# Performance work log

Measured on AMD Instinct MI355X. Metric: run time of the kernel, lower is better.

## Reference

```python
import jax, jax.numpy as jnp
import numpy as np

EPS = 1e-5
B, HD, LD, OD, E = 4, 256, 512, 256, 64  # E = out_dim // reduction
H, W, H2, W2 = 64, 64, 32, 32

def conv1x1(x, Wt, b=None):
    # x: [B,C,H,W], Wt: [O,C]
    y = jnp.einsum('bchw,oc->bohw', x, Wt)
    if b is not None:
        y = y + b[None, :, None, None]
    return y

def bn(x, s, bi, m, v):
    # eval-mode BatchNorm2d with running stats
    inv = (s / jnp.sqrt(v + EPS))[None, :, None, None]
    return (x - m[None, :, None, None]) * inv + bi[None, :, None, None]

def setup_inputs() -> dict:
    key = jax.random.key(0)
    ks = jax.random.split(key, 24)
    def n(k, shape, scale=0.05):
        return jax.random.normal(k, shape, dtype=jnp.float32) * scale
    inp = {
        'high_feat': jax.random.normal(ks[0], (B, HD, H, W), dtype=jnp.float32),
        'low_feat': jax.random.normal(ks[1], (B, LD, H2, W2), dtype=jnp.float32),
        'W_high': n(ks[2], (E, HD)),
        'bn_h_scale': 1.0 + n(ks[3], (E,)), 'bn_h_bias': n(ks[4], (E,)),
        'bn_h_mean': n(ks[5], (E,)), 'bn_h_var': 0.5 + jax.random.uniform(ks[6], (E,), dtype=jnp.float32),
        'W_low': n(ks[7], (E, LD)),
        'bn_l_scale': 1.0 + n(ks[8], (E,)), 'bn_l_bias': n(ks[9], (E,)),
        'bn_l_mean': n(ks[10], (E,)), 'bn_l_var': 0.5 + jax.random.uniform(ks[11], (E,), dtype=jnp.float32),
        'W_q': n(ks[12], (E, E)), 'b_q': n(ks[13], (E,)),
        'W_k': n(ks[14], (E, E)), 'b_k': n(ks[15], (E,)),
        'W_vh': n(ks[16], (OD, HD)), 'b_vh': n(ks[17], (OD,)),
        'W_vl': n(ks[18], (OD, LD)), 'b_vl': n(ks[19], (OD,)),
        'W_out': n(ks[20], (OD, 2 * OD)),
        'bn_o_scale': 1.0 + n(ks[21], (OD,)), 'bn_o_bias': n(ks[22], (OD,)),
        'bn_o_mean': jnp.zeros((OD,), jnp.float32), 'bn_o_var': jnp.ones((OD,), jnp.float32),
        'gamma': n(ks[23], (1,), scale=0.5),
    }
    return inp

def reference(high_feat, low_feat, W_high, bn_h_scale, bn_h_bias, bn_h_mean, bn_h_var,
              W_low, bn_l_scale, bn_l_bias, bn_l_mean, bn_l_var,
              W_q, b_q, W_k, b_k, W_vh, b_vh, W_vl, b_vl,
              W_out, bn_o_scale, bn_o_bias, bn_o_mean, bn_o_var, gamma):
    N = H * W
    # bilinear upsample low_feat to high_feat spatial size (align_corners=False)
    low = jax.image.resize(low_feat, (B, LD, H, W), method='bilinear')
    he = jax.nn.relu(bn(conv1x1(high_feat, W_high), bn_h_scale, bn_h_bias, bn_h_mean, bn_h_var))
    le = jax.nn.relu(bn(conv1x1(low, W_low), bn_l_scale, bn_l_bias, bn_l_mean, bn_l_var))
    q = conv1x1(he, W_q, b_q).reshape(B, E, N)   # [B,E,N1]
    k = conv1x1(le, W_k, b_k).reshape(B, E, N)   # [B,E,N2]
    energy = jnp.einsum('bcn,bcm->bnm', q, k)    # [B,N1,N2]
    attn = jax.nn.softmax(energy, axis=-1)
    vh = conv1x1(high_feat, W_vh, b_vh).reshape(B, OD, N)
    vl = conv1x1(low, W_vl, b_vl).reshape(B, OD, N)
    out_high = jnp.einsum('bcm,bnm->bcn', vh, attn).reshape(B, OD, H, W)
    out_low = jnp.einsum('bcn,bnm->bcm', vl, attn).reshape(B, OD, H, W)
    cat = jnp.concatenate([out_high, out_low], axis=1)  # [B,2*OD,H,W]
    out = jax.nn.relu(bn(conv1x1(cat, W_out), bn_o_scale, bn_o_bias, bn_o_mean, bn_o_var))
    return high_feat + gamma[0] * out
```

## Files before the change

### kernel.cpp

```cpp
#include <hip/hip_runtime.h>
#include <hip/hip_bf16.h>

#define B_   4
#define HD_  256
#define LD_  512
#define OD_  256
#define E_   64
#define N_   4096
#define N2_  1024
#define EPS_ 1e-5f

typedef __hip_bfloat16 bf16;
typedef __attribute__((ext_vector_type(8))) short short8;
typedef __attribute__((ext_vector_type(4))) float floatx4;

#define MFMA16(a, b, c) __builtin_amdgcn_mfma_f32_16x16x32_bf16(a, b, c, 0, 0, 0)

#define GLOAD(dst, ptr) \
  asm volatile("global_load_dwordx4 %0, %1, off" : "=v"(dst) : "v"(ptr) : "memory")
#define VWAIT() do { \
  asm volatile("s_waitcnt vmcnt(0)" ::: "memory"); \
  __builtin_amdgcn_sched_barrier(0); \
} while (0)

#define WH_OFF   0
#define WL_OFF   16384
#define WQ_OFF   49152
#define WK_OFF   53248
#define WVH_OFF  57344
#define WVL_OFF  122880
#define WO_OFF   253952
#define WTOT     385024

__device__ __forceinline__ unsigned short f2b_bits(float f) {
  union { float f; unsigned int u; } cv; cv.f = f;
  unsigned int u = cv.u;
  return (unsigned short)((u + 0x7FFFu + ((u >> 16) & 1u)) >> 16);
}
__device__ __forceinline__ float bits2f(unsigned short h) {
  union { unsigned int u; float f; } cv; cv.u = ((unsigned int)h) << 16;
  return cv.f;
}
__device__ __forceinline__ float ldext(const void* p, size_t i, int fl) {
  if (fl) return __bfloat162float(((const bf16*)p)[i]);
  return ((const float*)p)[i];
}
__device__ __forceinline__ short8 ld8(const short* p) { return *(const short8*)p; }
__device__ __forceinline__ short8 i4s8(int4 v) {
  union { int4 i; short8 s; } u; u.i = v; return u.s;
}
__device__ __forceinline__ short8 ldP(const unsigned short* row, int off) {
  ushort4 a = *(const ushort4*)(row + off);
  ushort4 b = *(const ushort4*)(row + off + 4);
  short8 r;
  r[0] = (short)a.x; r[1] = (short)a.y; r[2] = (short)a.z; r[3] = (short)a.w;
  r[4] = (short)b.x; r[5] = (short)b.y; r[6] = (short)b.z; r[7] = (short)b.w;
  return r;
}

__device__ __forceinline__ size_t frag_off(int r, int k, int K) {
  return ((size_t)(r >> 4) * ((size_t)K << 4)) + ((size_t)(k >> 5) << 9)
       + ((r & 15) << 5) + (k & 31);
}
__device__ __forceinline__ size_t v_off(int c, int m) {
  return ((size_t)(m >> 5) << 13) + ((c >> 4) << 9) + (((m >> 3) & 3) << 7)
       + ((c & 15) << 3) + (m & 7);
}

__global__ void detect_dtype_k(const void* probe, int* dflag) {
  if (threadIdx.x == 0 && blockIdx.x == 0) {
    const unsigned int* u = (const unsigned int*)probe;
    int bf = 1;
    for (int i = 0; i < 32; i++)
      if (u[i] != 0x3F803F80u) bf = 0;
    dflag[0] = bf;
  }
}

__global__ __launch_bounds__(256) void cvt_weights_k(
    const void* Wh, const void* Wl, const void* Wq, const void* Wk,
    const void* Wvh, const void* Wvl, const void* Wo,
    unsigned short* wbuf, const int* dflag)
{
  const int fl = dflag[0];
  int i = blockIdx.x * 256 + threadIdx.x;
  if (i >= WTOT) return;
  const void* src; int li, off, ksh;
  if      (i < WL_OFF)  { src = Wh;  li = i - WH_OFF;  off = WH_OFF;  ksh = 8; }
  else if (i < WQ_OFF)  { src = Wl;  li = i - WL_OFF;  off = WL_OFF;  ksh = 9; }
  else if (i < WK_OFF)  { src = Wq;  li = i - WQ_OFF;  off = WQ_OFF;  ksh = 6; }
  else if (i < WVH_OFF) { src = Wk;  li = i - WK_OFF;  off = WK_OFF;  ksh = 6; }
  else if (i < WVL_OFF) { src = Wvh; li = i - WVH_OFF; off = WVH_OFF; ksh = 8; }
  else if (i < WO_OFF)  { src = Wvl; li = i - WVL_OFF; off = WVL_OFF; ksh = 9; }
  else                  { src = Wo;  li = i - WO_OFF;  off = WO_OFF;  ksh = 9; }
  int K = 1 << ksh;
  int r = li >> ksh, k = li & (K - 1);
  wbuf[off + frag_off(r, k, K)] = f2b_bits(ldext(src, li, fl));
}

__global__ __launch_bounds__(256) void transpose_cvt_k(
    const void* X, unsigned short* Xt, int C, int S, const int* dflag)
{
  __shared__ unsigned short T[64][66];
  const int fl = dflag[0];
  const int tid = threadIdx.x;
  const int s0 = blockIdx.x * 64, c0 = blockIdx.y * 64, b = blockIdx.z;
  const size_t ibase = (size_t)b * C * S;
  const size_t obase = (size_t)b * S * C;
  const int sl = tid & 63, q = tid >> 6;
  for (int i = 0; i < 16; i++) {
    int c = q + i * 4;
    T[c][sl] = f2b_bits(ldext(X, ibase + (size_t)(c0 + c) * S + s0 + sl, fl));
  }
  __syncthreads();
  for (int i = 0; i < 16; i++) {
    int s = q + i * 4;
    Xt[obase + frag_off(s0 + s, c0 + sl, C)] = T[sl][s];
  }
}

__global__ __launch_bounds__(256) void gemm_k(
    const unsigned short* A, long sA,
    const unsigned short* Bm, long sB,
    unsigned short* D, long sD, int ldd,
    int K, int mode, int axis, int swz,
    const void* p0, const void* p1, const void* p2, const void* p3,
    const int* dflag)
{
  const int fl = dflag[0];
  const int tid = threadIdx.x;
  const int w = tid >> 6, lane = tid & 63;
  const int g = lane >> 4, c16 = lane & 15;
  const int r0 = blockIdx.x * 64 + (w >> 1) * 32;
  const int c0 = blockIdx.y * 64 + (w & 1) * 32;
  const short* Ab = (const short*)A + (size_t)blockIdx.z * sA;
  const short* Bb = (const short*)Bm + (size_t)blockIdx.z * sB;
  unsigned short* Db = D + (size_t)blockIdx.z * sD;

  floatx4 acc[2][2];
  #pragma unroll
  for (int i = 0; i < 2; i++)
    #pragma unroll
    for (int j = 0; j < 2; j++) acc[i][j] = (floatx4){0.f, 0.f, 0.f, 0.f};

  for (int k0 = 0; k0 < K; k0 += 64) {
    short8 Af[2][2], Bf[2][2];
    #pragma unroll
    for (int t = 0; t < 2; t++)
      #pragma unroll
      for (int kc = 0; kc < 2; kc++) {
        Af[t][kc] = ld8(Ab + frag_off(r0 + t * 16 + c16, k0 + kc * 32 + g * 8, K));
        Bf[t][kc] = ld8(Bb + frag_off(c0 + t * 16 + c16, k0 + kc * 32 + g * 8, K));
      }
    #pragma unroll
    for (int kc = 0; kc < 2; kc++)
      #pragma unroll
      for (int rt = 0; rt < 2; rt++)
        #pragma unroll
        for (int ct = 0; ct < 2; ct++)
          acc[rt][ct] = MFMA16(Af[rt][kc], Bf[ct][kc], acc[rt][ct]);
  }

  #pragma unroll
  for (int rt = 0; rt < 2; rt++)
    #pragma unroll
    for (int ct = 0; ct < 2; ct++)
      #pragma unroll
      for (int r = 0; r < 4; r++) {
        int rr = r0 + rt * 16 + g * 4 + r;
        int cc = c0 + ct * 16 + c16;
        int pi = axis ? rr : cc;
        float v = acc[rt][ct][r];
        if (mode == 1) v += ldext(p0, pi, fl);
        else if (mode >= 2) {
          float inv = ldext(p0, pi, fl) * rsqrtf(ldext(p3, pi, fl) + EPS_);
          v = v * inv + (ldext(p1, pi, fl) - ldext(p2, pi, fl) * inv);
          if (mode == 3) v = fmaxf(v, 0.f);
        }
        size_t idx;
        if (swz == 1)      idx = frag_off(rr, cc, ldd);
        else if (swz == 2) idx = v_off(rr, cc);
        else               idx = (size_t)rr * ldd + cc;
        Db[idx] = f2b_bits(v);
      }
}

__global__ __launch_bounds__(256) void upsample_rows_k(
    const unsigned short* src, unsigned short* dst, int relu)
{
  int idx = blockIdx.x * 256 + threadIdx.x;
  int e = idx & 63, n = (idx >> 6) & (N_ - 1), b = idx >> 18;
  int y = n >> 6, x = n & 63;
  int y0 = (y - 1) >> 1;  float wy = (y & 1) ? 0.25f : 0.75f;
  int x0 = (x - 1) >> 1;  float wx = (x & 1) ? 0.25f : 0.75f;
  int y0c = max(y0, 0), y1c = min(y0 + 1, 31);
  int x0c = max(x0, 0), x1c = min(x0 + 1, 31);
  const unsigned short* sb = src + ((size_t)b * N2_) * 64 + e;
  float v00 = bits2f(sb[(y0c * 32 + x0c) * 64]), v01 = bits2f(sb[(y0c * 32 + x1c) * 64]);
  float v10 = bits2f(sb[(y1c * 32 + x0c) * 64]), v11 = bits2f(sb[(y1c * 32 + x1c) * 64]);
  float v = (1.f - wy) * ((1.f - wx) * v00 + wx * v01)
          + wy * ((1.f - wx) * v10 + wx * v11);
  if (relu) v = fmaxf(v, 0.f);
  dst[(size_t)b * N_ * 64 + frag_off(n, e, 64)] = f2b_bits(v);
}

__global__ __launch_bounds__(256) void upsample_swz_k(
    const unsigned short* src, unsigned short* dst)
{
  int idx = blockIdx.x * 256 + threadIdx.x;
  int n = idx & (N_ - 1), c = (idx >> 12) & 255, b = idx >> 20;
  int y = n >> 6, x = n & 63;
  int y0 = (y - 1) >> 1;  float wy = (y & 1) ? 0.25f : 0.75f;
  int x0 = (x - 1) >> 1;  float wx = (x & 1) ? 0.25f : 0.75f;
  int y0c = max(y0, 0), y1c = min(y0 + 1, 31);
  int x0c = max(x0, 0), x1c = min(x0 + 1, 31);
  const unsigned short* sb = src + (size_t)(b * 256 + c) * N2_;
  float v00 = bits2f(sb[y0c * 32 + x0c]), v01 = bits2f(sb[y0c * 32 + x1c]);
  float v10 = bits2f(sb[y1c * 32 + x0c]), v11 = bits2f(sb[y1c * 32 + x1c]);
  float v = (1.f - wy) * ((1.f - wx) * v00 + wx * v01)
          + wy * ((1.f - wx) * v10 + wx * v11);
  dst[(size_t)b * 256 * N_ + v_off(c, n)] = f2b_bits(v);
}


__global__ __launch_bounds__(256, 4) void attn_apply_high_mfma_k(
    const bf16* qt, const bf16* kt, const bf16* vh,
    float* lsum_p, unsigned short* ohp0, unsigned short* ohp1)
{
  __shared__ __align__(16) unsigned short Pb[2][32][132];
  __shared__ float Lw[4][32];
  const int tid = threadIdx.x;
  const int w = tid >> 6, lane = tid & 63;
  const int g = lane >> 4, c16 = lane & 15;
  const int L = blockIdx.x;
  const int b = (L & 7) >> 1;
  const int n0 = (L >> 3) * 32;
  const int half = L & 1;
  const int mbase = half * 2048, mend = mbase + 2048;
  const short* q = (const short*)qt + (size_t)b * N_ * E_;
  const short* k = (const short*)kt + (size_t)b * N_ * E_;
  const short* v = (const short*)vh + (size_t)b * OD_ * N_;

  short8 Aq[2][2];
  #pragma unroll
  for (int nt = 0; nt < 2; nt++)
    #pragma unroll
    for (int ks = 0; ks < 2; ks++)
      Aq[nt][ks] = ld8(q + frag_off(n0 + nt * 16 + c16, ks * 32 + g * 8, 64));

  float lsum[2][4] = {};
  floatx4 oacc[2][4];
  #pragma unroll
  for (int nt = 0; nt < 2; nt++)
    #pragma unroll
    for (int ct = 0; ct < 4; ct++)
      oacc[nt][ct] = (floatx4){0.f, 0.f, 0.f, 0.f};

  short8 BkC[2][2];
  #pragma unroll
  for (int mt = 0; mt < 2; mt++)
    #pragma unroll
    for (int ks = 0; ks < 2; ks++)
      BkC[mt][ks] = ld8(k + frag_off(mbase + w * 32 + mt * 16 + c16, ks * 32 + g * 8, 64));

  int buf = 0;
  for (int m0 = mbase; m0 < mend; m0 += 128, buf ^= 1) {
    int4 bv[8];
    #pragma unroll
    for (int ks = 0; ks < 2; ks++)
      #pragma unroll
      for (int ct = 0; ct < 4; ct++)
        GLOAD(bv[ks * 4 + ct],
              (v + v_off(w * 64 + ct * 16 + c16, m0 + ks * 32 + g * 8)));
    floatx4 s[2][2];
    #pragma unroll
    for (int nt = 0; nt < 2; nt++)
      #pragma unroll
      for (int mt = 0; mt < 2; mt++) {
        floatx4 z = (floatx4){0.f, 0.f, 0.f, 0.f};
        z = MFMA16(Aq[nt][0], BkC[mt][0], z);
        z = MFMA16(Aq[nt][1], BkC[mt][1], z);
        s[nt][mt] = z;
      }
    int mn_ = m0 + 128;
    if (mn_ < mend) {
      #pragma unroll
      for (int mt = 0; mt < 2; mt++)
        #pragma unroll
        for (int ks = 0; ks < 2; ks++)
          BkC[mt][ks] = ld8(k + frag_off(mn_ + w * 32 + mt * 16 + c16, ks * 32 + g * 8, 64));
    }
    #pragma unroll
    for (int nt = 0; nt < 2; nt++)
      #pragma unroll
      for (int mt = 0; mt < 2; mt++)
        #pragma unroll
        for (int r = 0; r < 4; r++) {
          float p = __expf(fminf(s[nt][mt][r], 60.f));
          lsum[nt][r] += p;
          Pb[buf][nt * 16 + g * 4 + r][w * 32 + mt * 16 + c16] = f2b_bits(p);
        }
    __syncthreads();
    VWAIT();
    #pragma unroll
    for (int ks = 0; ks < 2; ks++) {
      short8 Ap0 = ldP(&Pb[buf][c16][0],      ks * 32 + g * 8);
      short8 Ap1 = ldP(&Pb[buf][16 + c16][0], ks * 32 + g * 8);
      #pragma unroll
      for (int ct = 0; ct < 4; ct++) {
        short8 Bv = i4s8(bv[ks * 4 + ct]);
        oacc[0][ct] = MFMA16(Ap0, Bv, oacc[0][ct]);
        oacc[1][ct] = MFMA16(Ap1, Bv, oacc[1][ct]);
      }
    }
    #pragma unroll
    for (int ks = 0; ks < 2; ks++)
      #pragma unroll
      for (int ct = 0; ct < 4; ct++)
        GLOAD(bv[ks * 4 + ct],
              (v + v_off(w * 64 + ct * 16 + c16, m0 + (ks + 2) * 32 + g * 8)));
    VWAIT();
    #pragma unroll
    for (int ks = 0; ks < 2; ks++) {
      short8 Ap0 = ldP(&Pb[buf][c16][0],      (ks + 2) * 32 + g * 8);
      short8 Ap1 = ldP(&Pb[buf][16 + c16][0], (ks + 2) * 32 + g * 8);
      #pragma unroll
      for (int ct = 0; ct < 4; ct++) {
        short8 Bv = i4s8(bv[ks * 4 + ct]);
        oacc[0][ct] = MFMA16(Ap0, Bv, oacc[0][ct]);
        oacc[1][ct] = MFMA16(Ap1, Bv, oacc[1][ct]);
      }
    }
  }
  #pragma unroll
  for (int d = 1; d < 16; d <<= 1)
    #pragma unroll
    for (int nt = 0; nt < 2; nt++)
      #pragma unroll
      for (int r = 0; r < 4; r++)
        lsum[nt][r] += __shfl_xor(lsum[nt][r], d);
  if (c16 == 0)
    #pragma unroll
    for (int nt = 0; nt < 2; nt++)
      #pragma unroll
      for (int r = 0; r < 4; r++)
        Lw[w][nt * 16 + g * 4 + r] = lsum[nt][r];
  __syncthreads();
  if (tid < 32)
    lsum_p[(size_t)half * 16384 + (size_t)b * N_ + n0 + tid] =
        Lw[0][tid] + Lw[1][tid] + Lw[2][tid] + Lw[3][tid];
  unsigned short* op = (half ? ohp1 : ohp0) + (size_t)b * N_ * OD_;
  #pragma unroll
  for (int nt = 0; nt < 2; nt++)
    #pragma unroll
    for (int ct = 0; ct < 4; ct++)
      #pragma unroll
      for (int r = 0; r < 4; r++) {
        int n = n0 + nt * 16 + g * 4 + r;
        int c = w * 64 + ct * 16 + c16;
        op[frag_off(n, c, 256)] = f2b_bits(oacc[nt][ct][r]);
      }
}

__global__ __launch_bounds__(256) void reduce_high_k(
    const unsigned short* p0, const unsigned short* p1, const float* lsum_p,
    unsigned short* oh, float* rsumG)
{
  size_t i8 = ((size_t)blockIdx.x * 256 + threadIdx.x) * 8;
  int slab = (int)(i8 >> 20);
  int loc  = (int)(i8 & 0xFFFFF);
  int n = (loc >> 12) * 16 + ((loc >> 5) & 15);
  int row = slab * N_ + n;
  float l = lsum_p[row] + lsum_p[16384 + row];
  float ri = 1.0f / l;
  const unsigned short* a = p0 + i8;
  const unsigned short* b = p1 + i8;
  short8 o;
  #pragma unroll
  for (int i = 0; i < 8; i++)
    o[i] = (short)f2b_bits((bits2f(a[i]) + bits2f(b[i])) * ri);
  *(short8*)(oh + i8) = o;
  if ((loc & 31) == 0) rsumG[row] = l;
}

__global__ __launch_bounds__(256, 4) void attn_apply_low_mfma_k(
    const bf16* qt, const bf16* kt, const bf16* vl,
    const float* rsumG, unsigned short* olp0, unsigned short* olp1)
{
  __shared__ __align__(16) unsigned short Pb[2][32][132];
  const int tid = threadIdx.x;
  const int w = tid >> 6, lane = tid & 63;
  const int g = lane >> 4, c16 = lane & 15;
  const int L = blockIdx.x;
  const int b = (L & 7) >> 1;
  const int m0 = (L >> 3) * 32;
  const int half = L & 1;
  const int nbase = half * 2048, nend = nbase + 2048;
  const short* q = (const short*)qt + (size_t)b * N_ * E_;
  const short* k = (const short*)kt + (size_t)b * N_ * E_;
  const short* v = (const short*)vl + (size_t)b * OD_ * N_;

  short8 Ak[2][2];
  #pragma unroll
  for (int mt = 0; mt < 2; mt++)
    #pragma unroll
    for (int ks = 0; ks < 2; ks++)
      Ak[mt][ks] = ld8(k + frag_off(m0 + mt * 16 + c16, ks * 32 + g * 8, 64));

  floatx4 oacc[2][4];
  #pragma unroll
  for (int mt = 0; mt < 2; mt++)
    #pragma unroll
    for (int ct = 0; ct < 4; ct++)
      oacc[mt][ct] = (floatx4){0.f, 0.f, 0.f, 0.f};

  short8 BqC[2][2];
  float riC[2];
  #pragma unroll
  for (int nt = 0; nt < 2; nt++) {
    #pragma unroll
    for (int ks = 0; ks < 2; ks++)
      BqC[nt][ks] = ld8(q + frag_off(nbase + w * 32 + nt * 16 + c16, ks * 32 + g * 8, 64));
    riC[nt] = 1.0f / rsumG[(size_t)b * N_ + nbase + w * 32 + nt * 16 + c16];
  }

  int buf = 0;
  for (int nL = nbase; nL < nend; nL += 128, buf ^= 1) {
    int4 bv[8];
    #pragma unroll
    for (int ks = 0; ks < 2; ks++)
      #pragma unroll
      for (int ct = 0; ct < 4; ct++)
        GLOAD(bv[ks * 4 + ct],
              (v + v_off(w * 64 + ct * 16 + c16, nL + ks * 32 + g * 8)));
    floatx4 s[2][2];
    #pragma unroll
    for (int mt = 0; mt < 2; mt++)
      #pragma unroll
      for (int nt = 0; nt < 2; nt++) {
        floatx4 z = (floatx4){0.f, 0.f, 0.f, 0.f};
        z = MFMA16(Ak[mt][0], BqC[nt][0], z);
        z = MFMA16(Ak[mt][1], BqC[nt][1], z);
        s[mt][nt] = z;
      }
    float riU[2]; riU[0] = riC[0]; riU[1] = riC[1];
    int nn_ = nL + 128;
    if (nn_ < nend) {
      #pragma unroll
      for (int nt = 0; nt < 2; nt++) {
        #pragma unroll
        for (int ks = 0; ks < 2; ks++)
          BqC[nt][ks] = ld8(q + frag_off(nn_ + w * 32 + nt * 16 + c16, ks * 32 + g * 8, 64));
        riC[nt] = 1.0f / rsumG[(size_t)b * N_ + nn_ + w * 32 + nt * 16 + c16];
      }
    }
    #pragma unroll
    for (int mt = 0; mt < 2; mt++)
      #pragma unroll
      for (int nt = 0; nt < 2; nt++)
        #pragma unroll
        for (int r = 0; r < 4; r++)
          Pb[buf][mt * 16 + g * 4 + r][w * 32 + nt * 16 + c16] =
              f2b_bits(__expf(fminf(s[mt][nt][r], 60.f)) * riU[nt]);
    __syncthreads();
    VWAIT();
    #pragma unroll
    for (int ks = 0; ks < 2; ks++) {
      short8 Ap0 = ldP(&Pb[buf][c16][0],      ks * 32 + g * 8);
      short8 Ap1 = ldP(&Pb[buf][16 + c16][0], ks * 32 + g * 8);
      #pragma unroll
      for (int ct = 0; ct < 4; ct++) {
        short8 Bv = i4s8(bv[ks * 4 + ct]);
        oacc[0][ct] = MFMA16(Ap0, Bv, oacc[0][ct]);
        oacc[1][ct] = MFMA16(Ap1, Bv, oacc[1][ct]);
      }
    }
    #pragma unroll
    for (int ks = 0; ks < 2; ks++)
      #pragma unroll
      for (int ct = 0; ct < 4; ct++)
        GLOAD(bv[ks * 4 + ct],
              (v + v_off(w * 64 + ct * 16 + c16, nL + (ks + 2) * 32 + g * 8)));
    VWAIT();
    #pragma unroll
    for (int ks = 0; ks < 2; ks++) {
      short8 Ap0 = ldP(&Pb[buf][c16][0],      (ks + 2) * 32 + g * 8);
      short8 Ap1 = ldP(&Pb[buf][16 + c16][0], (ks + 2) * 32 + g * 8);
      #pragma unroll
      for (int ct = 0; ct < 4; ct++) {
        short8 Bv = i4s8(bv[ks * 4 + ct]);
        oacc[0][ct] = MFMA16(Ap0, Bv, oacc[0][ct]);
        oacc[1][ct] = MFMA16(Ap1, Bv, oacc[1][ct]);
      }
    }
  }
  unsigned short* op = (half ? olp1 : olp0) + (size_t)b * N_ * OD_;
  #pragma unroll
  for (int mt = 0; mt < 2; mt++)
    #pragma unroll
    for (int ct = 0; ct < 4; ct++)
      #pragma unroll
      for (int r = 0; r < 4; r++) {
        int m = m0 + mt * 16 + g * 4 + r;
        int c = w * 64 + ct * 16 + c16;
        op[frag_off(m, c, 256)] = f2b_bits(oacc[mt][ct][r]);
      }
}

__global__ __launch_bounds__(256) void reduce_low_k(
    const unsigned short* p0, const unsigned short* p1, unsigned short* ol)
{
  size_t i8 = ((size_t)blockIdx.x * 256 + threadIdx.x) * 8;
  const unsigned short* a = p0 + i8;
  const unsigned short* b = p1 + i8;
  short8 o;
  #pragma unroll
  for (int i = 0; i < 8; i++)
    o[i] = (short)f2b_bits(bits2f(a[i]) + bits2f(b[i]));
  *(short8*)(ol + i8) = o;
}

__global__ __launch_bounds__(256) void final_mfma_k(
    const unsigned short* Wo, const unsigned short* oh, const unsigned short* ol,
    const void* sc, const void* bi, const void* mn, const void* vr,
    const void* hf, const void* gamma, void* out, const int* dflag)
{
  const int fl = dflag[0];
  const int tid = threadIdx.x;
  const int w = tid >> 6, lane = tid & 63;
  const int g = lane >> 4, c16 = lane & 15;
  const int r0 = blockIdx.x * 64 + (w >> 1) * 32;
  const int c0 = blockIdx.y * 64 + (w & 1) * 32;
  const int b = blockIdx.z;

  floatx4 acc[2][2];
  #pragma unroll
  for (int i = 0; i < 2; i++)
    #pragma unroll
    for (int j = 0; j < 2; j++) acc[i][j] = (floatx4){0.f, 0.f, 0.f, 0.f};

  #pragma unroll
  for (int half = 0; half < 2; half++) {
    const short* Bb = (const short*)(half ? ol : oh) + (size_t)b * N_ * 256;
    for (int k0 = 0; k0 < 256; k0 += 64) {
      short8 Af[2][2], Bf[2][2];
      #pragma unroll
      for (int t = 0; t < 2; t++)
        #pragma unroll
        for (int kc = 0; kc < 2; kc++) {
          Af[t][kc] = ld8((const short*)Wo + frag_off(r0 + t * 16 + c16,
                          half * 256 + k0 + kc * 32 + g * 8, 512));
          Bf[t][kc] = ld8(Bb + frag_off(c0 + t * 16 + c16, k0 + kc * 32 + g * 8, 256));
        }
      #pragma unroll
      for (int kc = 0; kc < 2; kc++)
        #pragma unroll
        for (int rt = 0; rt < 2; rt++)
          #pragma unroll
          for (int ct = 0; ct < 2; ct++)
            acc[rt][ct] = MFMA16(Af[rt][kc], Bf[ct][kc], acc[rt][ct]);
    }
  }

  float gm = ldext(gamma, 0, fl);
  #pragma unroll
  for (int rt = 0; rt < 2; rt++)
    #pragma unroll
    for (int r = 0; r < 4; r++) {
      int o = r0 + rt * 16 + g * 4 + r;
      float inv = ldext(sc, o, fl) * rsqrtf(ldext(vr, o, fl) + EPS_);
      float bb = ldext(bi, o, fl) - ldext(mn, o, fl) * inv;
      #pragma unroll
      for (int ct = 0; ct < 2; ct++) {
        int n = c0 + ct * 16 + c16;
        float v = acc[rt][ct][r] * inv + bb;
        v = fmaxf(v, 0.f);
        size_t idx = ((size_t)b * OD_ + o) * N_ + n;
        float res = ldext(hf, idx, fl) + gm * v;
        if (fl) ((bf16*)out)[idx] = __float2bfloat16(res);
        else    ((float*)out)[idx] = res;
      }
    }
}

extern "C" void kernel_launch(void* const* d_in, const int* in_sizes, int n_in,
                              void* d_out, int out_size, void* d_ws, size_t ws_size,
                              hipStream_t stream)
{
  const void* hf     = d_in[0];
  const void* lf     = d_in[1];
  const void* W_high = d_in[2];
  const void* bhs = d_in[3],  *bhb = d_in[4],  *bhm = d_in[5],  *bhv = d_in[6];
  const void* W_low  = d_in[7];
  const void* bls = d_in[8],  *blb = d_in[9],  *blm = d_in[10], *blv = d_in[11];
  const void* W_q    = d_in[12], *b_q = d_in[13];
  const void* W_k    = d_in[14], *b_k = d_in[15];
  const void* W_vh   = d_in[16], *b_vh = d_in[17];
  const void* W_vl   = d_in[18], *b_vl = d_in[19];
  const void* W_out  = d_in[20];
  const void* bos = d_in[21], *bob = d_in[22], *bom = d_in[23], *bov = d_in[24];
  const void* gamma  = d_in[25];

  char* wp = (char*)d_ws;
  int*   dflag  = (int*)wp;                                 wp += 64;
  float* rsum   = (float*)wp;                               wp += 16384 * 4;
  float* lsum_p = (float*)wp;                               wp += 2 * 16384 * 4;
  unsigned short* wbuf  = (unsigned short*)wp;              wp += WTOT * 2;
  unsigned short* hf_t  = (unsigned short*)wp;              wp += (size_t)B_ * N_ * 256 * 2;
  unsigned short* lf_t  = (unsigned short*)wp;              wp += (size_t)B_ * N2_ * 512 * 2;
  unsigned short* he_t  = (unsigned short*)wp;              wp += (size_t)B_ * N_ * 64 * 2;
  unsigned short* le_sm = (unsigned short*)wp;              wp += (size_t)B_ * N2_ * 64 * 2;
  unsigned short* le_t  = (unsigned short*)wp;              wp += (size_t)B_ * N_ * 64 * 2;
  unsigned short* vl_sm = (unsigned short*)wp;              wp += (size_t)B_ * 256 * N2_ * 2;
  unsigned short* vh    = (unsigned short*)wp;              wp += (size_t)B_ * 256 * N_ * 2;
  unsigned short* vl    = (unsigned short*)wp;              wp += (size_t)B_ * 256 * N_ * 2;
  unsigned short* ol    = (unsigned short*)wp;              wp += (size_t)B_ * N_ * 256 * 2;
  unsigned short* pext  = (unsigned short*)wp;              wp += (size_t)B_ * N_ * 256 * 2;
  unsigned short* oh = hf_t;
  unsigned short* qv = lf_t;
  unsigned short* kv = lf_t + (size_t)B_ * N_ * 64;
  unsigned short* ohp0 = ol;
  unsigned short* ohp1 = pext;
  unsigned short* olp0 = vh;
  unsigned short* olp1 = pext;

  dim3 blk(256);
  detect_dtype_k<<<1, 64, 0, stream>>>(bov, dflag);
  cvt_weights_k<<<WTOT / 256, blk, 0, stream>>>(W_high, W_low, W_q, W_k, W_vh, W_vl, W_out,
                                                wbuf, dflag);
  transpose_cvt_k<<<dim3(64, 4, B_), blk, 0, stream>>>(hf, hf_t, 256, N_, dflag);
  transpose_cvt_k<<<dim3(16, 8, B_), blk, 0, stream>>>(lf, lf_t, 512, N2_, dflag);

  gemm_k<<<dim3(256, 1, 1), blk, 0, stream>>>(hf_t, 0, wbuf + WH_OFF, 0,
      he_t, 0, 64, 256, 3, 0, 1, bhs, bhb, bhm, bhv, dflag);
  gemm_k<<<dim3(4, 64, B_), blk, 0, stream>>>(wbuf + WVH_OFF, 0,
      hf_t, (long)N_ * 256, vh, (long)256 * N_, N_, 256, 1, 1, 2,
      b_vh, b_vh, b_vh, b_vh, dflag);
  gemm_k<<<dim3(64, 1, 1), blk, 0, stream>>>(lf_t, 0, wbuf + WL_OFF, 0,
      le_sm, 0, 64, 512, 2, 0, 0, bls, blb, blm, blv, dflag);
  gemm_k<<<dim3(4, 16, B_), blk, 0, stream>>>(wbuf + WVL_OFF, 0,
      lf_t, (long)N2_ * 512, vl_sm, (long)256 * N2_, N2_, 512, 1, 1, 0,
      b_vl, b_vl, b_vl, b_vl, dflag);
  upsample_rows_k<<<(B_ * N_ * 64) / 256, blk, 0, stream>>>(le_sm, le_t, 1);
  upsample_swz_k <<<(B_ * 256 * N_) / 256, blk, 0, stream>>>(vl_sm, vl);
  gemm_k<<<dim3(256, 1, 1), blk, 0, stream>>>(he_t, 0, wbuf + WQ_OFF, 0,
      qv, 0, 64, 64, 1, 0, 1, b_q, b_q, b_q, b_q, dflag);
  gemm_k<<<dim3(256, 1, 1), blk, 0, stream>>>(le_t, 0, wbuf + WK_OFF, 0,
      kv, 0, 64, 64, 1, 0, 1, b_k, b_k, b_k, b_k, dflag);

  attn_apply_high_mfma_k<<<dim3(1024), blk, 0, stream>>>((const bf16*)qv, (const bf16*)kv,
      (const bf16*)vh, lsum_p, ohp0, ohp1);
  reduce_high_k<<<dim3(2048), blk, 0, stream>>>(ohp0, ohp1, lsum_p, oh, rsum);
  attn_apply_low_mfma_k <<<dim3(1024), blk, 0, stream>>>((const bf16*)qv, (const bf16*)kv,
      (const bf16*)vl, rsum, olp0, olp1);
  reduce_low_k<<<dim3(2048), blk, 0, stream>>>(olp0, olp1, ol);

  final_mfma_k<<<dim3(4, 64, B_), blk, 0, stream>>>(wbuf + WO_OFF, oh, ol,
      bos, bob, bom, bov, hf, gamma, d_out, dflag);
}
```

Baseline: 381.1 us.

## Swap MFMA operands to store P transposed with packed LDS writes, prescale vl

In both attention kernels the score MFMA operands are swapped, so each lane holds four consecutive columns of P. Those four values are written to shared memory as one packed ushort4 store instead of scalar stores, and the row stride is padded to 136 so the later short8 LDS reads are aligned 16-byte loads. The row-sum reduction drops from a 16-way to a 4-way shuffle. In the low kernel the per-row softmax normalisation is moved out of the inner loop into a separate vlscale_k pass that divides vl by the row sums beforehand, at the cost of an extra read and write over vl.

```diff
diff --git a/kernel.cpp b/kernel.cpp
--- a/kernel.cpp
+++ b/kernel.cpp
@@ -49,13 +49,8 @@
 __device__ __forceinline__ short8 i4s8(int4 v) {
   union { int4 i; short8 s; } u; u.i = v; return u.s;
 }
-__device__ __forceinline__ short8 ldP(const unsigned short* row, int off) {
-  ushort4 a = *(const ushort4*)(row + off);
-  ushort4 b = *(const ushort4*)(row + off + 4);
-  short8 r;
-  r[0] = (short)a.x; r[1] = (short)a.y; r[2] = (short)a.z; r[3] = (short)a.w;
-  r[4] = (short)b.x; r[5] = (short)b.y; r[6] = (short)b.z; r[7] = (short)b.w;
-  return r;
+__device__ __forceinline__ short8 ldP(const unsigned short* p) {
+  return *(const short8*)p;
 }
 
 __device__ __forceinline__ size_t frag_off(int r, int k, int K) {
@@ -227,7 +222,7 @@
     const bf16* qt, const bf16* kt, const bf16* vh,
     float* lsum_p, unsigned short* ohp0, unsigned short* ohp1)
 {
-  __shared__ __align__(16) unsigned short Pb[2][32][132];
+  __shared__ __align__(16) unsigned short Pb[2][32][136];
   __shared__ float Lw[4][32];
   const int tid = threadIdx.x;
   const int w = tid >> 6, lane = tid & 63;
@@ -241,14 +236,14 @@
   const short* k = (const short*)kt + (size_t)b * N_ * E_;
   const short* v = (const short*)vh + (size_t)b * OD_ * N_;
 
-  short8 Aq[2][2];
+  short8 Bq[2][2];
   #pragma unroll
   for (int nt = 0; nt < 2; nt++)
     #pragma unroll
     for (int ks = 0; ks < 2; ks++)
-      Aq[nt][ks] = ld8(q + frag_off(n0 + nt * 16 + c16, ks * 32 + g * 8, 64));
-
-  float lsum[2][4] = {};
+      Bq[nt][ks] = ld8(q + frag_off(n0 + nt * 16 + c16, ks * 32 + g * 8, 64));
+
+  float lsum[2] = {0.f, 0.f};
   floatx4 oacc[2][4];
   #pragma unroll
   for (int nt = 0; nt < 2; nt++)
@@ -256,12 +251,12 @@
     for (int ct = 0; ct < 4; ct++)
       oacc[nt][ct] = (floatx4){0.f, 0.f, 0.f, 0.f};
 
-  short8 BkC[2][2];
+  short8 Ak[2][2];
   #pragma unroll
   for (int mt = 0; mt < 2; mt++)
     #pragma unroll
     for (int ks = 0; ks < 2; ks++)
-      BkC[mt][ks] = ld8(k + frag_off(mbase + w * 32 + mt * 16 + c16, ks * 32 + g * 8, 64));
+      Ak[mt][ks] = ld8(k + frag_off(mbase + w * 32 + mt * 16 + c16, ks * 32 + g * 8, 64));
 
   int buf = 0;
   for (int m0 = mbase; m0 < mend; m0 += 128, buf ^= 1) {
@@ -274,13 +269,13 @@
               (v + v_off(w * 64 + ct * 16 + c16, m0 + ks * 32 + g * 8)));
     floatx4 s[2][2];
     #pragma unroll
-    for (int nt = 0; nt < 2; nt++)
-      #pragma unroll
-      for (int mt = 0; mt < 2; mt++) {
+    for (int mt = 0; mt < 2; mt++)
+      #pragma unroll
+      for (int nt = 0; nt < 2; nt++) {
         floatx4 z = (floatx4){0.f, 0.f, 0.f, 0.f};
-        z = MFMA16(Aq[nt][0], BkC[mt][0], z);
-        z = MFMA16(Aq[nt][1], BkC[mt][1], z);
-        s[nt][mt] = z;
+        z = MFMA16(Ak[mt][0], Bq[nt][0], z);
+        z = MFMA16(Ak[mt][1], Bq[nt][1], z);
+        s[mt][nt] = z;
       }
     int mn_ = m0 + 128;
     if (mn_ < mend) {
@@ -288,24 +283,28 @@
       for (int mt = 0; mt < 2; mt++)
         #pragma unroll
         for (int ks = 0; ks < 2; ks++)
-          BkC[mt][ks] = ld8(k + frag_off(mn_ + w * 32 + mt * 16 + c16, ks * 32 + g * 8, 64));
-    }
-    #pragma unroll
-    for (int nt = 0; nt < 2; nt++)
-      #pragma unroll
-      for (int mt = 0; mt < 2; mt++)
-        #pragma unroll
-        for (int r = 0; r < 4; r++) {
-          float p = __expf(fminf(s[nt][mt][r], 60.f));
-          lsum[nt][r] += p;
-          Pb[buf][nt * 16 + g * 4 + r][w * 32 + mt * 16 + c16] = f2b_bits(p);
-        }
+          Ak[mt][ks] = ld8(k + frag_off(mn_ + w * 32 + mt * 16 + c16, ks * 32 + g * 8, 64));
+    }
+    #pragma unroll
+    for (int mt = 0; mt < 2; mt++)
+      #pragma unroll
+      for (int nt = 0; nt < 2; nt++) {
+        ushort4 pk;
+        float p0v = __expf(fminf(s[mt][nt][0], 60.f));
+        float p1v = __expf(fminf(s[mt][nt][1], 60.f));
+        float p2v = __expf(fminf(s[mt][nt][2], 60.f));
+        float p3v = __expf(fminf(s[mt][nt][3], 60.f));
+        lsum[nt] += p0v + p1v + p2v + p3v;
+        pk.x = f2b_bits(p0v); pk.y = f2b_bits(p1v);
+        pk.z = f2b_bits(p2v); pk.w = f2b_bits(p3v);
+        *(ushort4*)&Pb[buf][nt * 16 + c16][w * 32 + mt * 16 + 4 * g] = pk;
+      }
     __syncthreads();
     VWAIT();
     #pragma unroll
     for (int ks = 0; ks < 2; ks++) {
-      short8 Ap0 = ldP(&Pb[buf][c16][0],      ks * 32 + g * 8);
-      short8 Ap1 = ldP(&Pb[buf][16 + c16][0], ks * 32 + g * 8);
+      short8 Ap0 = ldP(&Pb[buf][c16][ks * 32 + g * 8]);
+      short8 Ap1 = ldP(&Pb[buf][16 + c16][ks * 32 + g * 8]);
       #pragma unroll
       for (int ct = 0; ct < 4; ct++) {
         short8 Bv = i4s8(bv[ks * 4 + ct]);
@@ -322,8 +321,8 @@
     VWAIT();
     #pragma unroll
     for (int ks = 0; ks < 2; ks++) {
-      short8 Ap0 = ldP(&Pb[buf][c16][0],      (ks + 2) * 32 + g * 8);
-      short8 Ap1 = ldP(&Pb[buf][16 + c16][0], (ks + 2) * 32 + g * 8);
+      short8 Ap0 = ldP(&Pb[buf][c16][(ks + 2) * 32 + g * 8]);
+      short8 Ap1 = ldP(&Pb[buf][16 + c16][(ks + 2) * 32 + g * 8]);
       #pragma unroll
       for (int ct = 0; ct < 4; ct++) {
         short8 Bv = i4s8(bv[ks * 4 + ct]);
@@ -333,18 +332,14 @@
     }
   }
   #pragma unroll
-  for (int d = 1; d < 16; d <<= 1)
+  for (int nt = 0; nt < 2; nt++) {
+    lsum[nt] += __shfl_xor(lsum[nt], 16);
+    lsum[nt] += __shfl_xor(lsum[nt], 32);
+  }
+  if (g == 0)
     #pragma unroll
     for (int nt = 0; nt < 2; nt++)
-      #pragma unroll
-      for (int r = 0; r < 4; r++)
-        lsum[nt][r] += __shfl_xor(lsum[nt][r], d);
-  if (c16 == 0)
-    #pragma unroll
-    for (int nt = 0; nt < 2; nt++)
-      #pragma unroll
-      for (int r = 0; r < 4; r++)
-        Lw[w][nt * 16 + g * 4 + r] = lsum[nt][r];
+      Lw[w][nt * 16 + c16] = lsum[nt];
   __syncthreads();
   if (tid < 32)
     lsum_p[(size_t)half * 16384 + (size_t)b * N_ + n0 + tid] =
@@ -383,11 +378,27 @@
   if ((loc & 31) == 0) rsumG[row] = l;
 }
 
+__global__ __launch_bounds__(256) void vlscale_k(
+    unsigned short* vl, const float* rsumG)
+{
+  size_t i8 = ((size_t)blockIdx.x * 256 + threadIdx.x) * 8;
+  int b   = (int)(i8 >> 20);
+  int loc = (int)(i8 & 0xFFFFF);
+  int m0 = ((loc >> 13) << 5) + (((loc >> 7) & 3) << 3);
+  const float* rs = rsumG + (size_t)b * N_ + m0;
+  unsigned short* p = vl + i8;
+  short8 o;
+  #pragma unroll
+  for (int i = 0; i < 8; i++)
+    o[i] = (short)f2b_bits(bits2f(p[i]) / rs[i]);
+  *(short8*)p = o;
+}
+
 __global__ __launch_bounds__(256, 4) void attn_apply_low_mfma_k(
     const bf16* qt, const bf16* kt, const bf16* vl,
-    const float* rsumG, unsigned short* olp0, unsigned short* olp1)
-{
-  __shared__ __align__(16) unsigned short Pb[2][32][132];
+    unsigned short* olp0, unsigned short* olp1)
+{
+  __shared__ __align__(16) unsigned short Pb[2][32][136];
   const int tid = threadIdx.x;
   const int w = tid >> 6, lane = tid & 63;
   const int g = lane >> 4, c16 = lane & 15;
@@ -400,12 +411,12 @@
   const short* k = (const short*)kt + (size_t)b * N_ * E_;
   const short* v = (const short*)vl + (size_t)b * OD_ * N_;
 
-  short8 Ak[2][2];
+  short8 Bk[2][2];
   #pragma unroll
   for (int mt = 0; mt < 2; mt++)
     #pragma unroll
     for (int ks = 0; ks < 2; ks++)
-      Ak[mt][ks] = ld8(k + frag_off(m0 + mt * 16 + c16, ks * 32 + g * 8, 64));
+      Bk[mt][ks] = ld8(k + frag_off(m0 + mt * 16 + c16, ks * 32 + g * 8, 64));
 
   floatx4 oacc[2][4];
   #pragma unroll
@@ -414,15 +425,12 @@
     for (int ct = 0; ct < 4; ct++)
       oacc[mt][ct] = (floatx4){0.f, 0.f, 0.f, 0.f};
 
-  short8 BqC[2][2];
-  float riC[2];
-  #pragma unroll
-  for (int nt = 0; nt < 2; nt++) {
-    #pragma unroll
-    for (int ks = 0; ks < 2; ks++)
-      BqC[nt][ks] = ld8(q + frag_off(nbase + w * 32 + nt * 16 + c16, ks * 32 + g * 8, 64));
-    riC[nt] = 1.0f / rsumG[(size_t)b * N_ + nbase + w * 32 + nt * 16 + c16];
-  }
+  short8 Aq[2][2];
+  #pragma unroll
+  for (int nt = 0; nt < 2; nt++)
+    #pragma unroll
+    for (int ks = 0; ks < 2; ks++)
+      Aq[nt][ks] = ld8(q + frag_off(nbase + w * 32 + nt * 16 + c16, ks * 32 + g * 8, 64));
 
   int buf = 0;
   for (int nL = nbase; nL < nend; nL += 128, buf ^= 1) {
@@ -435,39 +443,39 @@
               (v + v_off(w * 64 + ct * 16 + c16, nL + ks * 32 + g * 8)));
     floatx4 s[2][2];
     #pragma unroll
-    for (int mt = 0; mt < 2; mt++)
-      #pragma unroll
-      for (int nt = 0; nt < 2; nt++) {
+    for (int nt = 0; nt < 2; nt++)
+      #pragma unroll
+      for (int mt = 0; mt < 2; mt++) {
         floatx4 z = (floatx4){0.f, 0.f, 0.f, 0.f};
-        z = MFMA16(Ak[mt][0], BqC[nt][0], z);
-        z = MFMA16(Ak[mt][1], BqC[nt][1], z);
-        s[mt][nt] = z;
-      }
-    float riU[2]; riU[0] = riC[0]; riU[1] = riC[1];
+        z = MFMA16(Aq[nt][0], Bk[mt][0], z);
+        z = MFMA16(Aq[nt][1], Bk[mt][1], z);
+        s[nt][mt] = z;
+      }
     int nn_ = nL + 128;
     if (nn_ < nend) {
       #pragma unroll
-      for (int nt = 0; nt < 2; nt++) {
+      for (int nt = 0; nt < 2; nt++)
         #pragma unroll
         for (int ks = 0; ks < 2; ks++)
-          BqC[nt][ks] = ld8(q + frag_off(nn_ + w * 32 + nt * 16 + c16, ks * 32 + g * 8, 64));
-        riC[nt] = 1.0f / rsumG[(size_t)b * N_ + nn_ + w * 32 + nt * 16 + c16];
-      }
-    }
-    #pragma unroll
-    for (int mt = 0; mt < 2; mt++)
-      #pragma unroll
-      for (int nt = 0; nt < 2; nt++)
-        #pragma unroll
-        for (int r = 0; r < 4; r++)
-          Pb[buf][mt * 16 + g * 4 + r][w * 32 + nt * 16 + c16] =
-              f2b_bits(__expf(fminf(s[mt][nt][r], 60.f)) * riU[nt]);
+          Aq[nt][ks] = ld8(q + frag_off(nn_ + w * 32 + nt * 16 + c16, ks * 32 + g * 8, 64));
+    }
+    #pragma unroll
+    for (int nt = 0; nt < 2; nt++)
+      #pragma unroll
+      for (int mt = 0; mt < 2; mt++) {
+        ushort4 pk;
+        pk.x = f2b_bits(__expf(fminf(s[nt][mt][0], 60.f)));
+        pk.y = f2b_bits(__expf(fminf(s[nt][mt][1], 60.f)));
+        pk.z = f2b_bits(__expf(fminf(s[nt][mt][2], 60.f)));
+        pk.w = f2b_bits(__expf(fminf(s[nt][mt][3], 60.f)));
+        *(ushort4*)&Pb[buf][mt * 16 + c16][w * 32 + nt * 16 + 4 * g] = pk;
+      }
     __syncthreads();
     VWAIT();
     #pragma unroll
     for (int ks = 0; ks < 2; ks++) {
-      short8 Ap0 = ldP(&Pb[buf][c16][0],      ks * 32 + g * 8);
-      short8 Ap1 = ldP(&Pb[buf][16 + c16][0], ks * 32 + g * 8);
+      short8 Ap0 = ldP(&Pb[buf][c16][ks * 32 + g * 8]);
+      short8 Ap1 = ldP(&Pb[buf][16 + c16][ks * 32 + g * 8]);
       #pragma unroll
       for (int ct = 0; ct < 4; ct++) {
         short8 Bv = i4s8(bv[ks * 4 + ct]);
@@ -484,8 +492,8 @@
     VWAIT();
     #pragma unroll
     for (int ks = 0; ks < 2; ks++) {
-      short8 Ap0 = ldP(&Pb[buf][c16][0],      (ks + 2) * 32 + g * 8);
-      short8 Ap1 = ldP(&Pb[buf][16 + c16][0], (ks + 2) * 32 + g * 8);
+      short8 Ap0 = ldP(&Pb[buf][c16][(ks + 2) * 32 + g * 8]);
+      short8 Ap1 = ldP(&Pb[buf][16 + c16][(ks + 2) * 32 + g * 8]);
       #pragma unroll
       for (int ct = 0; ct < 4; ct++) {
         short8 Bv = i4s8(bv[ks * 4 + ct]);
@@ -626,8 +634,8 @@
 
   dim3 blk(256);
   detect_dtype_k<<<1, 64, 0, stream>>>(bov, dflag);
-  cvt_weights_k<<<WTOT / 256, blk, 0, stream>>>(W_high, W_low, W_q, W_k, W_vh, W_vl, W_out,
-                                                wbuf, dflag);
+  cvt_weights_k<<<(WTOT + 255) / 256, blk, 0, stream>>>(W_high, W_low, W_q, W_k, W_vh, W_vl,
+                                                        W_out, wbuf, dflag);
   transpose_cvt_k<<<dim3(64, 4, B_), blk, 0, stream>>>(hf, hf_t, 256, N_, dflag);
   transpose_cvt_k<<<dim3(16, 8, B_), blk, 0, stream>>>(lf, lf_t, 512, N2_, dflag);
 
@@ -651,8 +659,9 @@
   attn_apply_high_mfma_k<<<dim3(1024), blk, 0, stream>>>((const bf16*)qv, (const bf16*)kv,
       (const bf16*)vh, lsum_p, ohp0, ohp1);
   reduce_high_k<<<dim3(2048), blk, 0, stream>>>(ohp0, ohp1, lsum_p, oh, rsum);
+  vlscale_k<<<dim3(2048), blk, 0, stream>>>(vl, rsum);
   attn_apply_low_mfma_k <<<dim3(1024), blk, 0, stream>>>((const bf16*)qv, (const bf16*)kv,
-      (const bf16*)vl, rsum, olp0, olp1);
+      (const bf16*)vl, olp0, olp1);
   reduce_low_k<<<dim3(2048), blk, 0, stream>>>(olp0, olp1, ol);
 
   final_mfma_k<<<dim3(4, 64, B_), blk, 0, stream>>>(wbuf + WO_OFF, oh, ol,
```

New measurement: 370.0 us. 2.9% less time.
